# Kernel optimization log

Hardware: AMD Instinct MI355X
Metric: run time of the kernel (lower is better)

The kernel has to match this reference:

```python
import jax, jax.numpy as jnp
import numpy as np

ALPHA = 1.0

def setup_inputs() -> dict:
    key = jax.random.key(0)
    k1, k2 = jax.random.split(key)
    x = jax.random.normal(k1, (131072, 512), dtype=jnp.float32)
    # xavier_uniform for (n_clusters, hidden_dim)
    n_clusters, hidden_dim = 512, 512
    limit = np.sqrt(6.0 / (n_clusters + hidden_dim))
    cluster_centers = jax.random.uniform(k2, (n_clusters, hidden_dim), dtype=jnp.float32, minval=-limit, maxval=limit)
    return {"x": x, "cluster_centers": cluster_centers}

def reference(x, cluster_centers):
    x2 = jnp.sum(x * x, axis=1, keepdims=True)            # (N, 1)
    c2 = jnp.sum(cluster_centers * cluster_centers, axis=1)  # (K,)
    dist2 = x2 + c2[None, :] - 2.0 * (x @ cluster_centers.T)  # (N, K)
    dist2 = jnp.maximum(dist2, 0.0)
    q = 1.0 / (1.0 + dist2 / ALPHA)
    q = q ** ((ALPHA + 1.0) / 2.0)
    q = q / jnp.sum(q, axis=1, keepdims=True)
    return q
```

## Files before the change

kernel.cpp:

```cpp
#include <hip/hip_runtime.h>


typedef __attribute__((ext_vector_type(8))) short short8_t;
typedef __attribute__((ext_vector_type(4))) short short4_t;
typedef __attribute__((ext_vector_type(4))) float f32x4;

#define NROWS 131072
#define DDIM  512
#define NCL   512
#define BK    32
#define MT    32
#define APAD  40

__device__ __forceinline__ unsigned short f2bf(float f) {
    unsigned u = __float_as_uint(f);
    u += 0x7FFFu + ((u >> 16) & 1u);
    return (unsigned short)(u >> 16);
}

__global__ __launch_bounds__(128) void prep_centers(
        const float* __restrict__ c, unsigned short* __restrict__ cb,
        float* __restrict__ c2) {
    const int k = blockIdx.x, t = threadIdx.x;
    float4 v = ((const float4*)(c + k * DDIM))[t];
    float ss = v.x * v.x + v.y * v.y + v.z * v.z + v.w * v.w;
    short4_t s;
    s.x = (short)f2bf(v.x); s.y = (short)f2bf(v.y);
    s.z = (short)f2bf(v.z); s.w = (short)f2bf(v.w);
    ((short4_t*)(cb + k * DDIM))[t] = s;
#pragma unroll
    for (int off = 32; off >= 1; off >>= 1) ss += __shfl_xor(ss, off, 64);
    __shared__ float red[2];
    if ((t & 63) == 0) red[t >> 6] = ss;
    __syncthreads();
    if (t == 0) c2[k] = red[0] + red[1];
}

__global__ __launch_bounds__(256, 3) void dec_soft_assign(
        const float* __restrict__ x, const unsigned short* __restrict__ cb,
        const float* __restrict__ c2g, float* __restrict__ out) {
    __shared__ __align__(16) unsigned short Alds[MT * APAD];
    __shared__ __align__(16) unsigned short Blds[NCL * BK];
    __shared__ float x2_lds[MT];
    __shared__ float rs_lds[MT][4];
    __shared__ float inv_lds[MT];

    const int t   = threadIdx.x;
    const int w   = t >> 6;
    const int l   = t & 63;
    const int q   = l >> 4;
    const int l15 = l & 15;
    const int m0  = blockIdx.x * MT;

    const int ar  = t >> 3;
    const int ac4 = t & 7;
    const float4* xp = (const float4*)(x + (m0 + ar) * DDIM) + ac4;

    int bgo[8];
#pragma unroll
    for (int i = 0; i < 8; ++i) {
        int cl = i * 256 + t;
        int n  = cl >> 2;
        int cp = cl & 3;
        int cc = cp ^ ((n >> 1) & 3);
        bgo[i] = n * DDIM + cc * 8;
    }

    f32x4 acc[2][8];
#pragma unroll
    for (int mt = 0; mt < 2; ++mt)
#pragma unroll
        for (int nt = 0; nt < 8; ++nt)
            acc[mt][nt] = (f32x4){0.f, 0.f, 0.f, 0.f};

    float x2a = 0.f;
    float4 av = xp[0];

    for (int kt = 0; kt < 16; ++kt) {
        __syncthreads();
        x2a += av.x * av.x + av.y * av.y + av.z * av.z + av.w * av.w;
        short4_t a4;
        a4.x = (short)f2bf(av.x); a4.y = (short)f2bf(av.y);
        a4.z = (short)f2bf(av.z); a4.w = (short)f2bf(av.w);
        *(short4_t*)&Alds[ar * APAD + ac4 * 4] = a4;
#pragma unroll
        for (int i = 0; i < 8; ++i) {
            __builtin_amdgcn_global_load_lds(
                (const __attribute__((address_space(1))) void*)(cb + bgo[i] + kt * BK),
                (__attribute__((address_space(3))) void*)&Blds[(i * 256 + w * 64) * 8],
                16, 0, 0);
        }
        __syncthreads();
        if (kt < 15) av = xp[(kt + 1) * 8];

        short8_t afr[2], bfr[8];
#pragma unroll
        for (int mt = 0; mt < 2; ++mt)
            afr[mt] = *(const short8_t*)&Alds[(mt * 16 + l15) * APAD + q * 8];
#pragma unroll
        for (int nt = 0; nt < 8; ++nt) {
            int n  = w * 128 + nt * 16 + l15;
            int pc = q ^ ((n >> 1) & 3);
            bfr[nt] = *(const short8_t*)&Blds[n * BK + pc * 8];
        }
#pragma unroll
        for (int nt = 0; nt < 8; ++nt) {
            acc[0][nt] = __builtin_amdgcn_mfma_f32_16x16x32_bf16(afr[0], bfr[nt], acc[0][nt], 0, 0, 0);
            acc[1][nt] = __builtin_amdgcn_mfma_f32_16x16x32_bf16(afr[1], bfr[nt], acc[1][nt], 0, 0, 0);
        }
    }

    x2a += __shfl_xor(x2a, 1, 64);
    x2a += __shfl_xor(x2a, 2, 64);
    x2a += __shfl_xor(x2a, 4, 64);
    if (ac4 == 0) x2_lds[ar] = x2a;
    __syncthreads();

    float c2v[8];
#pragma unroll
    for (int nt = 0; nt < 8; ++nt)
        c2v[nt] = c2g[w * 128 + nt * 16 + l15];

    float rsum[2][4];
#pragma unroll
    for (int mt = 0; mt < 2; ++mt)
#pragma unroll
        for (int r = 0; r < 4; ++r) rsum[mt][r] = 0.f;

#pragma unroll
    for (int mt = 0; mt < 2; ++mt) {
#pragma unroll
        for (int r = 0; r < 4; ++r) {
            float xv = x2_lds[mt * 16 + q * 4 + r];
#pragma unroll
            for (int nt = 0; nt < 8; ++nt) {
                float d = xv + c2v[nt] - 2.0f * acc[mt][nt][r];
                d = fmaxf(d, 0.0f);
                float qq = __builtin_amdgcn_rcpf(1.0f + d);
                acc[mt][nt][r] = qq;
                rsum[mt][r] += qq;
            }
        }
    }
#pragma unroll
    for (int mt = 0; mt < 2; ++mt)
#pragma unroll
        for (int r = 0; r < 4; ++r) {
            float s = rsum[mt][r];
            s += __shfl_xor(s, 1, 64);
            s += __shfl_xor(s, 2, 64);
            s += __shfl_xor(s, 4, 64);
            s += __shfl_xor(s, 8, 64);
            if (l15 == 0) rs_lds[mt * 16 + q * 4 + r][w] = s;
        }
    __syncthreads();
    if (t < MT) {
        float s = rs_lds[t][0] + rs_lds[t][1] + rs_lds[t][2] + rs_lds[t][3];
        inv_lds[t] = __builtin_amdgcn_rcpf(s);
    }
    __syncthreads();

#pragma unroll
    for (int mt = 0; mt < 2; ++mt)
#pragma unroll
        for (int r = 0; r < 4; ++r) {
            int row = mt * 16 + q * 4 + r;
            float inv = inv_lds[row];
            float* orow = out + (long)(m0 + row) * NCL + w * 128;
#pragma unroll
            for (int nt = 0; nt < 8; ++nt)
                orow[nt * 16 + l15] = acc[mt][nt][r] * inv;
        }
}

extern "C" void kernel_launch(void* const* d_in, const int* in_sizes, int n_in,
                              void* d_out, int out_size, void* d_ws, size_t ws_size,
                              hipStream_t stream) {
    const float* x       = (const float*)d_in[0];
    const float* centers = (const float*)d_in[1];
    float* out           = (float*)d_out;

    unsigned short* cb = (unsigned short*)d_ws;
    float* c2          = (float*)((char*)d_ws + NCL * DDIM * sizeof(unsigned short));

    prep_centers<<<NCL, 128, 0, stream>>>(centers, cb, c2);
    dec_soft_assign<<<NROWS / MT, 256, 0, stream>>>(x, cb, c2, out);
}
```

Measured before the change: 564.9 us.

## Double row tile to 64 rows per block to reuse center tiles

Raises the per-block row tile from 32 to 64, so each workgroup issues four A fragments per k-step and reuses every B (centers) fragment across 4 MFMAs instead of 2. Each thread now loads two float4s of x per step and writes a short8 into LDS, with padding reduced to 36. The goal is to halve the redundant center-tile loads from global/L2 and LDS per output row. In exchange, per-thread accumulator registers double and the launch bound drops to 2 blocks per SM, which reduces occupancy and latency hiding. Padding 36 may add LDS bank conflicts or misalign the 16-byte short8 accesses.

```diff
diff --git a/kernel.cpp b/kernel.cpp
--- a/kernel.cpp
+++ b/kernel.cpp
@@ -9,8 +9,8 @@
 #define DDIM  512
 #define NCL   512
 #define BK    32
-#define MT    32
-#define APAD  40
+#define MT    64
+#define APAD  36
 
 __device__ __forceinline__ unsigned short f2bf(float f) {
     unsigned u = __float_as_uint(f);
@@ -36,7 +36,7 @@
     if (t == 0) c2[k] = red[0] + red[1];
 }
 
-__global__ __launch_bounds__(256, 3) void dec_soft_assign(
+__global__ __launch_bounds__(256, 2) void dec_soft_assign(
         const float* __restrict__ x, const unsigned short* __restrict__ cb,
         const float* __restrict__ c2g, float* __restrict__ out) {
     __shared__ __align__(16) unsigned short Alds[MT * APAD];
@@ -52,9 +52,9 @@
     const int l15 = l & 15;
     const int m0  = blockIdx.x * MT;
 
-    const int ar  = t >> 3;
-    const int ac4 = t & 7;
-    const float4* xp = (const float4*)(x + (m0 + ar) * DDIM) + ac4;
+    const int ar  = t >> 2;
+    const int acj = t & 3;
+    const float4* xp = (const float4*)(x + (long)(m0 + ar) * DDIM) + acj * 2;
 
     int bgo[8];
 #pragma unroll
@@ -66,23 +66,26 @@
         bgo[i] = n * DDIM + cc * 8;
     }
 
-    f32x4 acc[2][8];
+    f32x4 acc[4][8];
 #pragma unroll
-    for (int mt = 0; mt < 2; ++mt)
+    for (int mt = 0; mt < 4; ++mt)
 #pragma unroll
         for (int nt = 0; nt < 8; ++nt)
             acc[mt][nt] = (f32x4){0.f, 0.f, 0.f, 0.f};
 
     float x2a = 0.f;
-    float4 av = xp[0];
+    float4 av0 = xp[0], av1 = xp[1];
 
     for (int kt = 0; kt < 16; ++kt) {
         __syncthreads();
-        x2a += av.x * av.x + av.y * av.y + av.z * av.z + av.w * av.w;
-        short4_t a4;
-        a4.x = (short)f2bf(av.x); a4.y = (short)f2bf(av.y);
-        a4.z = (short)f2bf(av.z); a4.w = (short)f2bf(av.w);
-        *(short4_t*)&Alds[ar * APAD + ac4 * 4] = a4;
+        x2a += av0.x * av0.x + av0.y * av0.y + av0.z * av0.z + av0.w * av0.w;
+        x2a += av1.x * av1.x + av1.y * av1.y + av1.z * av1.z + av1.w * av1.w;
+        short8_t a8;
+        a8[0] = (short)f2bf(av0.x); a8[1] = (short)f2bf(av0.y);
+        a8[2] = (short)f2bf(av0.z); a8[3] = (short)f2bf(av0.w);
+        a8[4] = (short)f2bf(av1.x); a8[5] = (short)f2bf(av1.y);
+        a8[6] = (short)f2bf(av1.z); a8[7] = (short)f2bf(av1.w);
+        *(short8_t*)&Alds[ar * APAD + acj * 8] = a8;
 #pragma unroll
         for (int i = 0; i < 8; ++i) {
             __builtin_amdgcn_global_load_lds(
@@ -91,11 +94,11 @@
                 16, 0, 0);
         }
         __syncthreads();
-        if (kt < 15) av = xp[(kt + 1) * 8];
+        if (kt < 15) { av0 = xp[(kt + 1) * 8]; av1 = xp[(kt + 1) * 8 + 1]; }
 
-        short8_t afr[2], bfr[8];
+        short8_t afr[4], bfr[8];
 #pragma unroll
-        for (int mt = 0; mt < 2; ++mt)
+        for (int mt = 0; mt < 4; ++mt)
             afr[mt] = *(const short8_t*)&Alds[(mt * 16 + l15) * APAD + q * 8];
 #pragma unroll
         for (int nt = 0; nt < 8; ++nt) {
@@ -104,16 +107,15 @@
             bfr[nt] = *(const short8_t*)&Blds[n * BK + pc * 8];
         }
 #pragma unroll
-        for (int nt = 0; nt < 8; ++nt) {
-            acc[0][nt] = __builtin_amdgcn_mfma_f32_16x16x32_bf16(afr[0], bfr[nt], acc[0][nt], 0, 0, 0);
-            acc[1][nt] = __builtin_amdgcn_mfma_f32_16x16x32_bf16(afr[1], bfr[nt], acc[1][nt], 0, 0, 0);
-        }
+        for (int nt = 0; nt < 8; ++nt)
+#pragma unroll
+            for (int mt = 0; mt < 4; ++mt)
+                acc[mt][nt] = __builtin_amdgcn_mfma_f32_16x16x32_bf16(afr[mt], bfr[nt], acc[mt][nt], 0, 0, 0);
     }
 
     x2a += __shfl_xor(x2a, 1, 64);
     x2a += __shfl_xor(x2a, 2, 64);
-    x2a += __shfl_xor(x2a, 4, 64);
-    if (ac4 == 0) x2_lds[ar] = x2a;
+    if (acj == 0) x2_lds[ar] = x2a;
     __syncthreads();
 
     float c2v[8];
@@ -121,14 +123,14 @@
     for (int nt = 0; nt < 8; ++nt)
         c2v[nt] = c2g[w * 128 + nt * 16 + l15];
 
-    float rsum[2][4];
+    float rsum[4][4];
 #pragma unroll
-    for (int mt = 0; mt < 2; ++mt)
+    for (int mt = 0; mt < 4; ++mt)
 #pragma unroll
         for (int r = 0; r < 4; ++r) rsum[mt][r] = 0.f;
 
 #pragma unroll
-    for (int mt = 0; mt < 2; ++mt) {
+    for (int mt = 0; mt < 4; ++mt) {
 #pragma unroll
         for (int r = 0; r < 4; ++r) {
             float xv = x2_lds[mt * 16 + q * 4 + r];
@@ -143,7 +145,7 @@
         }
     }
 #pragma unroll
-    for (int mt = 0; mt < 2; ++mt)
+    for (int mt = 0; mt < 4; ++mt)
 #pragma unroll
         for (int r = 0; r < 4; ++r) {
             float s = rsum[mt][r];
@@ -161,7 +163,7 @@
     __syncthreads();
 
 #pragma unroll
-    for (int mt = 0; mt < 2; ++mt)
+    for (int mt = 0; mt < 4; ++mt)
 #pragma unroll
         for (int r = 0; r < 4; ++r) {
             int row = mt * 16 + q * 4 + r;
```

Measured after the change: 504.0 us. -10.8%, faster.
